# Optimization experiments

Measured on AMD Instinct MI355X. Metric: run time of the kernel, lower is better.

Reference implementation:

```python
import jax, jax.numpy as jnp
import numpy as np

B, IN_CHAN, L = 16, 16, 4096
OUTC, KS = 64, 7

def _conv1d(x, w, b, stride=1, pad=0):
    # x: (N, Cin, L), w: (Cout, Cin, K)
    y = jax.lax.conv_general_dilated(x, w, (stride,), [(pad, pad)],
                                     dimension_numbers=('NCH', 'OIH', 'NCH'))
    return y + b[None, :, None]

def setup_inputs() -> dict:
    key = jax.random.key(0)
    ks = jax.random.split(key, 7)
    x = jax.random.normal(ks[0], (B, 1, L, IN_CHAN), dtype=jnp.float32)
    # offset-predicting conv (inc=1 -> KS offsets), k=3 pad=1
    p_w = jax.random.normal(ks[1], (KS, 1, 3), dtype=jnp.float32) * 0.1
    p_b = jax.random.normal(ks[2], (KS,), dtype=jnp.float32) * 0.1
    # modulation conv (inc=1 -> KS masks), k=3 pad=1
    m_w = jax.random.normal(ks[3], (KS, 1, 3), dtype=jnp.float32) * 0.1
    m_b = jax.random.normal(ks[4], (KS,), dtype=jnp.float32) * 0.1
    # main conv over resampled signal: (1 -> OUTC), k=KS, stride=KS
    c_w = jax.random.normal(ks[5], (OUTC, 1, KS), dtype=jnp.float32) * (1.0 / np.sqrt(KS))
    c_b = jax.random.normal(ks[6], (OUTC,), dtype=jnp.float32) * 0.1
    return {"x": x, "p_w": p_w, "p_b": p_b, "m_w": m_w, "m_b": m_b,
            "c_w": c_w, "c_b": c_b}

def _deform_conv1d(xs, p_w, p_b, m_w, m_b, c_w, c_b):
    # xs: (N, 1, L) single-channel 1D signal; returns (N, OUTC, L)
    N, _, Lx = xs.shape
    ksz = c_w.shape[2]
    offset = _conv1d(xs, p_w, p_b, pad=1)              # (N, ks, L)
    m = jax.nn.sigmoid(_conv1d(xs, m_w, m_b, pad=1))   # (N, ks, L)
    p_n = jnp.arange(-(ksz - 1) // 2, (ksz - 1) // 2 + 1, dtype=xs.dtype)  # kernel offsets
    p_0 = jnp.arange(1, Lx + 1, dtype=xs.dtype)        # base grid (starts at 1, as in deform-conv-v2)
    p = p_0[None, None, :] + p_n[None, :, None] + offset  # (N, ks, L)
    p = jnp.transpose(p, (0, 2, 1))                       # (N, L, ks)
    q_lt = jnp.clip(jnp.floor(jax.lax.stop_gradient(p)), 0, Lx - 1)
    q_rb = jnp.clip(q_lt + 1, 0, Lx - 1)
    p = jnp.clip(p, 0, Lx - 1)
    g_lt = 1 + (q_lt - p)                               # linear-interp weights
    g_rb = 1 - (q_rb - p)
    sig = xs[:, 0, :]                                   # (N, L) since inc == 1
    idx_lt = q_lt.astype(jnp.int32).reshape(N, Lx * ksz)
    idx_rb = q_rb.astype(jnp.int32).reshape(N, Lx * ksz)
    x_lt = jnp.take_along_axis(sig, idx_lt, axis=1).reshape(N, Lx, ksz)
    x_rb = jnp.take_along_axis(sig, idx_rb, axis=1).reshape(N, Lx, ksz)
    x_off = (g_lt * x_lt + g_rb * x_rb) * jnp.transpose(m, (0, 2, 1))  # (N, L, ks)
    x_off = x_off.reshape(N, 1, Lx * ksz)
    return _conv1d(x_off, c_w, c_b, stride=ksz)         # (N, OUTC, L)

def reference(x, p_w, p_b, m_w, m_b, c_w, c_b):
    # x: (B, 1, L, C); same DeformConv1D applied independently to every last-dim slice.
    # Fold the slice loop into the batch dim (same math, no Python loop).
    Bx, _, Lx, Cx = x.shape
    xs = jnp.transpose(x, (0, 3, 1, 2)).reshape(Bx * Cx, 1, Lx)
    y = _deform_conv1d(xs, p_w, p_b, m_w, m_b, c_w, c_b)  # (B*C, OUTC, L)
    y = y.reshape(Bx, Cx, -1, Lx)
    return jnp.transpose(y, (0, 2, 3, 1))                 # (B, OUTC, L, C)
```

## Files before the change

### kernel.cpp

```cpp
#include <hip/hip_runtime.h>
#include <math.h>

#define BB   16
#define CC   16
#define LL   4096
#define OUTC 64
#define KS   7

typedef float vfloat4 __attribute__((ext_vector_type(4)));

__global__ __launch_bounds__(256) void deform_conv_kernel(
    const float* __restrict__ x,
    const float* __restrict__ p_w,
    const float* __restrict__ p_b,
    const float* __restrict__ m_w,
    const float* __restrict__ m_b,
    const float* __restrict__ c_w,
    const float* __restrict__ c_b,
    float* __restrict__ out)
{
    __shared__ float cw_lds[OUTC * 8];
    __shared__ float pw_lds[KS * 4];
    __shared__ float mw_lds[KS * 4];

    const int tid = threadIdx.x;

    for (int i = tid; i < OUTC * 8; i += 256) {
        int o = i >> 3, j = i & 7;
        cw_lds[i] = (j < 7) ? c_w[o * 7 + j] : c_b[o];
    }
    if (tid < KS * 4) {
        int k = tid >> 2, j = tid & 3;
        pw_lds[tid] = (j < 3) ? p_w[k * 3 + j] : p_b[k];
        mw_lds[tid] = (j < 3) ? m_w[k * 3 + j] : m_b[k];
    }
    __syncthreads();

    const int b     = blockIdx.x >> 6;
    const int ltile = blockIdx.x & 63;
    const int cg    = tid & 3;
    const int l     = ltile * 64 + (tid >> 2);
    const int c0    = cg * 4;

    const float* xb = x + b * (LL * CC);

    float s_m1[4] = {0.f, 0.f, 0.f, 0.f};
    float s_p1[4] = {0.f, 0.f, 0.f, 0.f};
    float s_0[4];
    {
        float4 v0 = *(const float4*)(xb + l * CC + c0);
        s_0[0] = v0.x; s_0[1] = v0.y; s_0[2] = v0.z; s_0[3] = v0.w;
        if (l > 0) {
            float4 vm = *(const float4*)(xb + (l - 1) * CC + c0);
            s_m1[0] = vm.x; s_m1[1] = vm.y; s_m1[2] = vm.z; s_m1[3] = vm.w;
        }
        if (l < LL - 1) {
            float4 vp = *(const float4*)(xb + (l + 1) * CC + c0);
            s_p1[0] = vp.x; s_p1[1] = vp.y; s_p1[2] = vp.z; s_p1[3] = vp.w;
        }
    }

    float xoff[4][KS];
    const float pl = (float)(l + 1);
    #pragma unroll
    for (int k = 0; k < KS; ++k) {
        float4 pw = *(const float4*)(pw_lds + k * 4);
        float4 mw = *(const float4*)(mw_lds + k * 4);
        const float pn = (float)(k - 3);
        #pragma unroll
        for (int c = 0; c < 4; ++c) {
            float off  = pw.w + pw.x * s_m1[c] + pw.y * s_0[c] + pw.z * s_p1[c];
            float mact = mw.w + mw.x * s_m1[c] + mw.y * s_0[c] + mw.z * s_p1[c];
            float mm   = 1.f / (1.f + __expf(-mact));

            float p    = pl + pn + off;
            float qltf = fminf(fmaxf(floorf(p), 0.f), (float)(LL - 1));
            float qrbf = fminf(qltf + 1.f, (float)(LL - 1));
            float pc   = fminf(fmaxf(p, 0.f), (float)(LL - 1));
            float glt  = 1.f + (qltf - pc);
            float grb  = 1.f - (qrbf - pc);

            int ilt = (int)qltf;
            int irb = (int)qrbf;
            float xlt = xb[ilt * CC + c0 + c];
            float xrb = xb[irb * CC + c0 + c];

            xoff[c][k] = (glt * xlt + grb * xrb) * mm;
        }
    }

    float* outp = out + ((size_t)(b * OUTC) * LL + l) * CC + c0;
    #pragma unroll 4
    for (int o = 0; o < OUTC; ++o) {
        float4 w0 = *(const float4*)(cw_lds + o * 8);
        float4 w1 = *(const float4*)(cw_lds + o * 8 + 4);
        float acc[4];
        #pragma unroll
        for (int c = 0; c < 4; ++c) {
            float a = w1.w;
            a += w0.x * xoff[c][0];
            a += w0.y * xoff[c][1];
            a += w0.z * xoff[c][2];
            a += w0.w * xoff[c][3];
            a += w1.x * xoff[c][4];
            a += w1.y * xoff[c][5];
            a += w1.z * xoff[c][6];
            acc[c] = a;
        }
        vfloat4 res;
        res.x = acc[0]; res.y = acc[1]; res.z = acc[2]; res.w = acc[3];
        __builtin_nontemporal_store(res, (vfloat4*)(outp + (size_t)o * (LL * CC)));
    }
}

extern "C" void kernel_launch(void* const* d_in, const int* in_sizes, int n_in,
                              void* d_out, int out_size, void* d_ws, size_t ws_size,
                              hipStream_t stream) {
    const float* x   = (const float*)d_in[0];
    const float* p_w = (const float*)d_in[1];
    const float* p_b = (const float*)d_in[2];
    const float* m_w = (const float*)d_in[3];
    const float* m_b = (const float*)d_in[4];
    const float* c_w = (const float*)d_in[5];
    const float* c_b = (const float*)d_in[6];
    float* out = (float*)d_out;

    deform_conv_kernel<<<dim3(BB * 64), dim3(256), 0, stream>>>(
        x, p_w, p_b, m_w, m_b, c_w, c_b, out);
}
```

Before: 292.7 us.

## Transpose input to channel-major workspace and halve channels per thread

Adds a transpose kernel that writes x into a (B, C, L) workspace, so the gather for the two interpolation neighbours reads adjacent addresses along L instead of stride-16 scattered loads. The main kernel now handles 2 channels per thread instead of 4, doubling the grid, and declares a launch-bounds occupancy hint. The output stores become 8-byte nontemporal writes instead of 16-byte ones. The cost is an extra kernel launch and a full read-and-write pass over the input, plus narrower output stores. The fallback path runs when no workspace is provided.

```diff
diff --git a/kernel.cpp b/kernel.cpp
--- a/kernel.cpp
+++ b/kernel.cpp
@@ -7,16 +7,43 @@
 #define OUTC 64
 #define KS   7
 
+typedef float vfloat2 __attribute__((ext_vector_type(2)));
 typedef float vfloat4 __attribute__((ext_vector_type(4)));
 
-__global__ __launch_bounds__(256) void deform_conv_kernel(
+__global__ __launch_bounds__(256) void transpose_kernel(
+    const float* __restrict__ x, float* __restrict__ xT)
+{
+    __shared__ float tile[64 * 17];
+    const int b   = blockIdx.x >> 6;
+    const int l0  = (blockIdx.x & 63) * 64;
+    const int tid = threadIdx.x;
+    {
+        const int lo = tid >> 2, cq = (tid & 3) * 4;
+        float4 v = *(const float4*)(x + ((size_t)(b * LL + l0 + lo)) * CC + cq);
+        tile[lo * 17 + cq + 0] = v.x;
+        tile[lo * 17 + cq + 1] = v.y;
+        tile[lo * 17 + cq + 2] = v.z;
+        tile[lo * 17 + cq + 3] = v.w;
+    }
+    __syncthreads();
+    {
+        const int c = tid >> 4, li = (tid & 15) * 4;
+        float4 v;
+        v.x = tile[(li + 0) * 17 + c];
+        v.y = tile[(li + 1) * 17 + c];
+        v.z = tile[(li + 2) * 17 + c];
+        v.w = tile[(li + 3) * 17 + c];
+        *(float4*)(xT + ((size_t)(b * CC + c)) * LL + l0 + li) = v;
+    }
+}
+
+template <bool USE_XT>
+__global__ __launch_bounds__(256, 6) void deform_conv_kernel(
     const float* __restrict__ x,
-    const float* __restrict__ p_w,
-    const float* __restrict__ p_b,
-    const float* __restrict__ m_w,
-    const float* __restrict__ m_b,
-    const float* __restrict__ c_w,
-    const float* __restrict__ c_b,
+    const float* __restrict__ xT,
+    const float* __restrict__ p_w, const float* __restrict__ p_b,
+    const float* __restrict__ m_w, const float* __restrict__ m_b,
+    const float* __restrict__ c_w, const float* __restrict__ c_b,
     float* __restrict__ out)
 {
     __shared__ float cw_lds[OUTC * 8];
@@ -36,39 +63,39 @@
     }
     __syncthreads();
 
-    const int b     = blockIdx.x >> 6;
-    const int ltile = blockIdx.x & 63;
-    const int cg    = tid & 3;
-    const int l     = ltile * 64 + (tid >> 2);
-    const int c0    = cg * 4;
+    const int b     = blockIdx.x >> 7;
+    const int ltile = blockIdx.x & 127;
+    const int l     = ltile * 32 + (tid >> 3);
+    const int c0    = (tid & 7) * 2;
 
-    const float* xb = x + b * (LL * CC);
+    const float* xb = x + (size_t)b * (LL * CC);
 
-    float s_m1[4] = {0.f, 0.f, 0.f, 0.f};
-    float s_p1[4] = {0.f, 0.f, 0.f, 0.f};
-    float s_0[4];
+    float s_m1[2] = {0.f, 0.f};
+    float s_p1[2] = {0.f, 0.f};
+    float s_0[2];
     {
-        float4 v0 = *(const float4*)(xb + l * CC + c0);
-        s_0[0] = v0.x; s_0[1] = v0.y; s_0[2] = v0.z; s_0[3] = v0.w;
+        float2 v0 = *(const float2*)(xb + l * CC + c0);
+        s_0[0] = v0.x; s_0[1] = v0.y;
         if (l > 0) {
-            float4 vm = *(const float4*)(xb + (l - 1) * CC + c0);
-            s_m1[0] = vm.x; s_m1[1] = vm.y; s_m1[2] = vm.z; s_m1[3] = vm.w;
+            float2 vm = *(const float2*)(xb + (l - 1) * CC + c0);
+            s_m1[0] = vm.x; s_m1[1] = vm.y;
         }
         if (l < LL - 1) {
-            float4 vp = *(const float4*)(xb + (l + 1) * CC + c0);
-            s_p1[0] = vp.x; s_p1[1] = vp.y; s_p1[2] = vp.z; s_p1[3] = vp.w;
+            float2 vp = *(const float2*)(xb + (l + 1) * CC + c0);
+            s_p1[0] = vp.x; s_p1[1] = vp.y;
         }
     }
 
-    float xoff[4][KS];
+    float xoff[2][KS];
     const float pl = (float)(l + 1);
+    const float* xt0 = USE_XT ? (xT + (size_t)(b * CC + c0) * LL) : nullptr;
     #pragma unroll
     for (int k = 0; k < KS; ++k) {
         float4 pw = *(const float4*)(pw_lds + k * 4);
         float4 mw = *(const float4*)(mw_lds + k * 4);
         const float pn = (float)(k - 3);
         #pragma unroll
-        for (int c = 0; c < 4; ++c) {
+        for (int c = 0; c < 2; ++c) {
             float off  = pw.w + pw.x * s_m1[c] + pw.y * s_0[c] + pw.z * s_p1[c];
             float mact = mw.w + mw.x * s_m1[c] + mw.y * s_0[c] + mw.z * s_p1[c];
             float mm   = 1.f / (1.f + __expf(-mact));
@@ -80,11 +107,20 @@
             float glt  = 1.f + (qltf - pc);
             float grb  = 1.f - (qrbf - pc);
 
-            int ilt = (int)qltf;
-            int irb = (int)qrbf;
-            float xlt = xb[ilt * CC + c0 + c];
-            float xrb = xb[irb * CC + c0 + c];
-
+            float xlt, xrb;
+            if (USE_XT) {
+                int iload = (int)fminf(qltf, (float)(LL - 2));
+                const float* pr = xt0 + (size_t)c * LL + iload;
+                float va = pr[0];
+                float vb = pr[1];
+                xlt = (qltf >= (float)(LL - 1)) ? vb : va;
+                xrb = vb;
+            } else {
+                int ilt = (int)qltf;
+                int irb = (int)qrbf;
+                xlt = xb[ilt * CC + c0 + c];
+                xrb = xb[irb * CC + c0 + c];
+            }
             xoff[c][k] = (glt * xlt + grb * xrb) * mm;
         }
     }
@@ -94,9 +130,9 @@
     for (int o = 0; o < OUTC; ++o) {
         float4 w0 = *(const float4*)(cw_lds + o * 8);
         float4 w1 = *(const float4*)(cw_lds + o * 8 + 4);
-        float acc[4];
+        vfloat2 res;
         #pragma unroll
-        for (int c = 0; c < 4; ++c) {
+        for (int c = 0; c < 2; ++c) {
             float a = w1.w;
             a += w0.x * xoff[c][0];
             a += w0.y * xoff[c][1];
@@ -105,11 +141,9 @@
             a += w1.x * xoff[c][4];
             a += w1.y * xoff[c][5];
             a += w1.z * xoff[c][6];
-            acc[c] = a;
+            res[c] = a;
         }
-        vfloat4 res;
-        res.x = acc[0]; res.y = acc[1]; res.z = acc[2]; res.w = acc[3];
-        __builtin_nontemporal_store(res, (vfloat4*)(outp + (size_t)o * (LL * CC)));
+        __builtin_nontemporal_store(res, (vfloat2*)(outp + (size_t)o * (LL * CC)));
     }
 }
 
@@ -125,6 +159,14 @@
     const float* c_b = (const float*)d_in[6];
     float* out = (float*)d_out;
 
-    deform_conv_kernel<<<dim3(BB * 64), dim3(256), 0, stream>>>(
-        x, p_w, p_b, m_w, m_b, c_w, c_b, out);
+    const size_t xt_bytes = (size_t)BB * CC * LL * sizeof(float);
+    if (d_ws != nullptr && ws_size >= xt_bytes) {
+        float* xT = (float*)d_ws;
+        transpose_kernel<<<dim3(BB * 64), dim3(256), 0, stream>>>(x, xT);
+        deform_conv_kernel<true><<<dim3(BB * 128), dim3(256), 0, stream>>>(
+            x, xT, p_w, p_b, m_w, m_b, c_w, c_b, out);
+    } else {
+        deform_conv_kernel<false><<<dim3(BB * 128), dim3(256), 0, stream>>>(
+            x, nullptr, p_w, p_b, m_w, m_b, c_w, c_b, out);
+    }
 }
```

Measured after the change: 300.0 us. 2.5% more time.
